# Optimization experiments

Measured on AMD Instinct MI355X. Metric: run time of the kernel, lower is better.

## Reference

```python
import jax, jax.numpy as jnp
import numpy as np

SIGMA = 1.0


def _pairwise_max(q, fact_emb):
    # q: [B, N, D], fact_emb: [F, D]  (D = 3E)
    # Gaussian RBF kernel k(x,y) = exp(-||x-y||^2 / (2*sigma^2)), then max over F.
    q2 = jnp.sum(q * q, axis=-1, keepdims=True)            # [B, N, 1]
    f2 = jnp.sum(fact_emb * fact_emb, axis=-1)             # [F]
    qf = jnp.einsum('bnd,fd->bnf', q, fact_emb)            # [B, N, F]
    d2 = jnp.maximum(q2 + f2[None, None, :] - 2.0 * qf, 0.0)
    k = jnp.exp(-d2 / (2.0 * SIGMA ** 2))                  # [B, N, F]
    return jnp.max(k, axis=2)                              # [B, N]


def setup_inputs() -> dict:
    key = jax.random.key(0)
    ks = jax.random.split(key, 7)
    B, N, F, E = 8, 4000, 4000, 100
    return {
        'rel': jax.random.normal(ks[0], (B, E), jnp.float32),
        'arg1': jax.random.normal(ks[1], (B, E), jnp.float32),
        'arg2': jax.random.normal(ks[2], (B, E), jnp.float32),
        'fact_rel': jax.random.normal(ks[3], (F, E), jnp.float32),
        'fact_arg1': jax.random.normal(ks[4], (F, E), jnp.float32),
        'fact_arg2': jax.random.normal(ks[5], (F, E), jnp.float32),
        'entity_embeddings': jax.random.normal(ks[6], (N, E), jnp.float32),
    }


def reference(rel, arg1, arg2, fact_rel, fact_arg1, fact_arg2, entity_embeddings):
    B = rel.shape[0]
    N, E = entity_embeddings.shape
    fact_emb = jnp.concatenate([fact_rel, fact_arg1, fact_arg2], axis=1)  # [F, 3E]

    rel_b = jnp.broadcast_to(rel[:, None, :], (B, N, E))
    emb_b = jnp.broadcast_to(entity_embeddings[None, :, :], (B, N, E))

    # score_sp: query = [rel, arg1, entity]
    arg1_b = jnp.broadcast_to(arg1[:, None, :], (B, N, E))
    q_sp = jnp.concatenate([rel_b, arg1_b, emb_b], axis=2)  # [B, N, 3E]
    score_sp = _pairwise_max(q_sp, fact_emb)                # [B, N]

    # score_po: query = [rel, entity, arg2]
    arg2_b = jnp.broadcast_to(arg2[:, None, :], (B, N, E))
    q_po = jnp.concatenate([rel_b, emb_b, arg2_b], axis=2)  # [B, N, 3E]
    score_po = _pairwise_max(q_po, fact_emb)                # [B, N]

    return (score_sp, score_po)
```

## Files before the change

### kernel.cpp

```cpp
#include <hip/hip_runtime.h>
#include <math.h>

#define EDIM 100
#define KP   128
#define NF   4000
#define NN   4000
#define NB   8
#define NP   4096
#define BN   128
#define BF   64
#define NFB  (NP / BF)
#define TRS  68

typedef __attribute__((ext_vector_type(8))) short short8;
typedef __attribute__((ext_vector_type(4))) float floatx4;

__device__ __align__(16) unsigned short g_A [NP * KP];
__device__ __align__(16) unsigned short g_B1[NP * KP];
__device__ __align__(16) unsigned short g_B2[NP * KP];
__device__ __align__(16) float g_P[2 * NB * NP];
__device__ float g_e2[NN];
__device__ float g_part[2 * NB * NFB * NP];

__device__ __forceinline__ unsigned short f2bf(float x) {
    union { float f; unsigned int u; } v; v.f = x;
    unsigned int r = v.u + 0x7FFFu + ((v.u >> 16) & 1u);
    return (unsigned short)(r >> 16);
}

__global__ void convert(const float* __restrict__ ent,
                        const float* __restrict__ fa1,
                        const float* __restrict__ fa2) {
    int idx = blockIdx.x * 256 + threadIdx.x;
    const float* src = (blockIdx.y == 0) ? ent : (blockIdx.y == 1) ? fa1 : fa2;
    unsigned short* dst = (blockIdx.y == 0) ? g_A : (blockIdx.y == 1) ? g_B1 : g_B2;
    int row = idx >> 7, k = idx & (KP - 1);
    float v = (row < NF && k < EDIM) ? src[row * EDIM + k] : 0.f;
    dst[idx] = f2bf(v);
}

__global__ void precompute_P(const float* __restrict__ rel,
                             const float* __restrict__ arg1,
                             const float* __restrict__ arg2,
                             const float* __restrict__ frel,
                             const float* __restrict__ fa1,
                             const float* __restrict__ fa2) {
    const int t = threadIdx.x;
    const int fl = t & 15;
    const int kq = t >> 4;
    const int f = blockIdx.x * 16 + fl;
    const int b = blockIdx.y;
    const int fr = (f < NF) ? f : (NF - 1);

    float nf = 0.f, dr = 0.f, d1 = 0.f, d2 = 0.f, qr = 0.f, q1 = 0.f, q2 = 0.f;
    for (int i = 0; i < 25; i++) {
        int k = kq * 25 + i;
        float vr = frel[fr * EDIM + k];
        float v1 = fa1[fr * EDIM + k];
        float v2 = fa2[fr * EDIM + k];
        float rb = rel[b * EDIM + k];
        float a1 = arg1[b * EDIM + k];
        float a2 = arg2[b * EDIM + k];
        nf += vr * vr + v1 * v1 + v2 * v2;
        dr = fmaf(rb, vr, dr);
        d1 = fmaf(a1, v1, d1);
        d2 = fmaf(a2, v2, d2);
        qr = fmaf(rb, rb, qr);
        q1 = fmaf(a1, a1, q1);
        q2 = fmaf(a2, a2, q2);
    }
    nf += __shfl_xor(nf, 16); nf += __shfl_xor(nf, 32);
    dr += __shfl_xor(dr, 16); dr += __shfl_xor(dr, 32);
    d1 += __shfl_xor(d1, 16); d1 += __shfl_xor(d1, 32);
    d2 += __shfl_xor(d2, 16); d2 += __shfl_xor(d2, 32);
    qr += __shfl_xor(qr, 16); qr += __shfl_xor(qr, 32);
    q1 += __shfl_xor(q1, 16); q1 += __shfl_xor(q1, 32);
    q2 += __shfl_xor(q2, 16); q2 += __shfl_xor(q2, 32);
    if (kq == 0) {
        float psp = nf + qr + q1 - 2.f * (dr + d1);
        float ppo = nf + qr + q2 - 2.f * (dr + d2);
        if (f >= NF) { psp = __builtin_inff(); ppo = __builtin_inff(); }
        g_P[(0 * NB + b) * NP + f] = psp;
        g_P[(1 * NB + b) * NP + f] = ppo;
    }
}

__global__ void precompute_e2(const float* __restrict__ ent) {
    int n = blockIdx.x * 256 + threadIdx.x;
    if (n >= NN) return;
    const float4* ep = (const float4*)(ent + n * EDIM);
    float s = 0.f;
    #pragma unroll
    for (int i = 0; i < EDIM / 4; i++) {
        float4 v = ep[i];
        s += v.x * v.x + v.y * v.y + v.z * v.z + v.w * v.w;
    }
    g_e2[n] = s;
}

__global__ void __launch_bounds__(256, 2) main_kernel() {
    __shared__ float4 smem4[4352];
    float4* lA4  = smem4;
    float4* lB14 = smem4 + 2048;
    float4* lB24 = smem4 + 3072;
    float*  tr   = (float*)smem4;

    const int t = threadIdx.x;
    const int n0 = blockIdx.x * BN;
    const int fblk = blockIdx.y;
    const int f0 = fblk * BF;

    const float4* gA4 = (const float4*)g_A;
    const float4* gB14 = (const float4*)g_B1;
    const float4* gB24 = (const float4*)g_B2;
    #pragma unroll
    for (int i = 0; i < 8; i++) {
        int gc = i * 256 + t;
        int row = gc >> 4, ch = gc & 15;
        lA4[row * 16 + (ch ^ (row & 15))] = gA4[n0 * 16 + gc];
    }
    #pragma unroll
    for (int i = 0; i < 4; i++) {
        int gc = i * 256 + t;
        int row = gc >> 4, ch = gc & 15;
        int sl = row * 16 + (ch ^ (row & 15));
        lB14[sl] = gB14[f0 * 16 + gc];
        lB24[sl] = gB24[f0 * 16 + gc];
    }
    __syncthreads();

    const int lane = t & 63;
    const int c = lane & 15;
    const int q = lane >> 4;
    const int w = t >> 6;
    const int w32 = w * 32;

    const short8* pA  = (const short8*)lA4;
    const short8* pB1 = (const short8*)lB14;
    const short8* pB2 = (const short8*)lB24;

    floatx4 acc[2][2][4];
    #pragma unroll
    for (int g = 0; g < 2; g++)
        #pragma unroll
        for (int mt = 0; mt < 2; mt++)
            #pragma unroll
            for (int ft = 0; ft < 4; ft++)
                acc[g][mt][ft] = (floatx4){0.f, 0.f, 0.f, 0.f};

    #pragma unroll
    for (int s = 0; s < 4; s++) {
        const int base = s * 4 + q;
        short8 a0 = pA[(w32 + c) * 16 + (base ^ c)];
        short8 a1 = pA[(w32 + 16 + c) * 16 + (base ^ c)];
        #pragma unroll
        for (int ft = 0; ft < 4; ft++) {
            int sl = (ft * 16 + c) * 16 + (base ^ c);
            short8 b1 = pB1[sl];
            short8 b2 = pB2[sl];
            acc[0][0][ft] = __builtin_amdgcn_mfma_f32_16x16x32_bf16(a0, b2, acc[0][0][ft], 0, 0, 0);
            acc[0][1][ft] = __builtin_amdgcn_mfma_f32_16x16x32_bf16(a1, b2, acc[0][1][ft], 0, 0, 0);
            acc[1][0][ft] = __builtin_amdgcn_mfma_f32_16x16x32_bf16(a0, b1, acc[1][0][ft], 0, 0, 0);
            acc[1][1][ft] = __builtin_amdgcn_mfma_f32_16x16x32_bf16(a1, b1, acc[1][1][ft], 0, 0, 0);
        }
    }

    __syncthreads();

    #pragma unroll
    for (int g = 0; g < 2; g++)
        #pragma unroll
        for (int mt = 0; mt < 2; mt++)
            #pragma unroll
            for (int ft = 0; ft < 4; ft++)
                #pragma unroll
                for (int r = 0; r < 4; r++)
                    tr[(g * BN + w32 + mt * 16 + q * 4 + r) * TRS + ft * 16 + c] =
                        acc[g][mt][ft][r];
    __syncthreads();

    const int g2 = t >> 7;
    const int row = t & 127;
    const float4* trg = (const float4*)(tr + (g2 * BN + row) * TRS);
    float4 G4[16];
    #pragma unroll
    for (int ch = 0; ch < 16; ch++) G4[ch] = trg[ch];

    #pragma unroll
    for (int b = 0; b < NB; b++) {
        const float4* Pp = (const float4*)(g_P + (g2 * NB + b) * NP + f0);
        float4 m4 = {__builtin_inff(), __builtin_inff(), __builtin_inff(), __builtin_inff()};
        #pragma unroll
        for (int ch = 0; ch < 16; ch++) {
            float4 p = Pp[ch];
            m4.x = fminf(m4.x, fmaf(-2.f, G4[ch].x, p.x));
            m4.y = fminf(m4.y, fmaf(-2.f, G4[ch].y, p.y));
            m4.z = fminf(m4.z, fmaf(-2.f, G4[ch].z, p.z));
            m4.w = fminf(m4.w, fmaf(-2.f, G4[ch].w, p.w));
        }
        float m = fminf(fminf(m4.x, m4.y), fminf(m4.z, m4.w));
        g_part[((g2 * NB + b) * NFB + fblk) * NP + n0 + row] = m;
    }
}

__global__ void finalize(float* __restrict__ out) {
    int idx = blockIdx.x * 256 + threadIdx.x;
    if (idx >= 2 * NB * NN) return;
    int sb = idx / NN;
    int n = idx % NN;
    float m = __builtin_inff();
    #pragma unroll 8
    for (int j = 0; j < NFB; j++) m = fminf(m, g_part[(sb * NFB + j) * NP + n]);
    float d2 = fmaxf(m + g_e2[n], 0.f);
    out[idx] = expf(-0.5f * d2);
}

extern "C" void kernel_launch(void* const* d_in, const int* in_sizes, int n_in,
                              void* d_out, int out_size, void* d_ws, size_t ws_size,
                              hipStream_t stream) {
    const float* rel  = (const float*)d_in[0];
    const float* arg1 = (const float*)d_in[1];
    const float* arg2 = (const float*)d_in[2];
    const float* frel = (const float*)d_in[3];
    const float* fa1  = (const float*)d_in[4];
    const float* fa2  = (const float*)d_in[5];
    const float* ent  = (const float*)d_in[6];
    float* out = (float*)d_out;

    convert<<<dim3(NP * KP / 256, 3), 256, 0, stream>>>(ent, fa1, fa2);
    precompute_P<<<dim3(NP / 16, NB), 64, 0, stream>>>(rel, arg1, arg2, frel, fa1, fa2);
    precompute_e2<<<(NN + 255) / 256, 256, 0, stream>>>(ent);
    main_kernel<<<dim3(NP / BN, NFB), 256, 0, stream>>>();
    finalize<<<(2 * NB * NN + 255) / 256, 256, 0, stream>>>(out);
}
```

Before: 136.4 us.

## Fuse prep kernels and loop four F-blocks per main kernel block

The three preprocessing kernels are merged into a single launch that dispatches on block index, which removes two launches. Each main_kernel block now iterates over four F tiles and keeps running minima in registers. This cuts the partial-result buffer and the finalize reduction by a factor of four and stages the P values in shared memory. It still reloads the A tile every iteration, and the grid is four times smaller, which may lower occupancy and parallelism.

```diff
diff --git a/kernel.cpp b/kernel.cpp
--- a/kernel.cpp
+++ b/kernel.cpp
@@ -10,7 +10,13 @@
 #define BN   128
 #define BF   64
 #define NFB  (NP / BF)
+#define FPB  4
+#define NYB  (NFB / FPB)
 #define TRS  68
+
+#define CONVB (3 * (NP * KP / 256))
+#define PREPB ((NP / 64) * NB)
+#define E2B   ((NN + 255) / 256)
 
 typedef __attribute__((ext_vector_type(8))) short short8;
 typedef __attribute__((ext_vector_type(4))) float floatx4;
@@ -20,7 +26,7 @@
 __device__ __align__(16) unsigned short g_B2[NP * KP];
 __device__ __align__(16) float g_P[2 * NB * NP];
 __device__ float g_e2[NN];
-__device__ float g_part[2 * NB * NFB * NP];
+__device__ float g_part[2 * NB * NYB * NP];
 
 __device__ __forceinline__ unsigned short f2bf(float x) {
     union { float f; unsigned int u; } v; v.f = x;
@@ -28,78 +34,81 @@
     return (unsigned short)(r >> 16);
 }
 
-__global__ void convert(const float* __restrict__ ent,
-                        const float* __restrict__ fa1,
-                        const float* __restrict__ fa2) {
-    int idx = blockIdx.x * 256 + threadIdx.x;
-    const float* src = (blockIdx.y == 0) ? ent : (blockIdx.y == 1) ? fa1 : fa2;
-    unsigned short* dst = (blockIdx.y == 0) ? g_A : (blockIdx.y == 1) ? g_B1 : g_B2;
-    int row = idx >> 7, k = idx & (KP - 1);
-    float v = (row < NF && k < EDIM) ? src[row * EDIM + k] : 0.f;
-    dst[idx] = f2bf(v);
-}
-
-__global__ void precompute_P(const float* __restrict__ rel,
-                             const float* __restrict__ arg1,
-                             const float* __restrict__ arg2,
-                             const float* __restrict__ frel,
-                             const float* __restrict__ fa1,
-                             const float* __restrict__ fa2) {
-    const int t = threadIdx.x;
-    const int fl = t & 15;
-    const int kq = t >> 4;
-    const int f = blockIdx.x * 16 + fl;
-    const int b = blockIdx.y;
-    const int fr = (f < NF) ? f : (NF - 1);
-
-    float nf = 0.f, dr = 0.f, d1 = 0.f, d2 = 0.f, qr = 0.f, q1 = 0.f, q2 = 0.f;
-    for (int i = 0; i < 25; i++) {
-        int k = kq * 25 + i;
-        float vr = frel[fr * EDIM + k];
-        float v1 = fa1[fr * EDIM + k];
-        float v2 = fa2[fr * EDIM + k];
-        float rb = rel[b * EDIM + k];
-        float a1 = arg1[b * EDIM + k];
-        float a2 = arg2[b * EDIM + k];
-        nf += vr * vr + v1 * v1 + v2 * v2;
-        dr = fmaf(rb, vr, dr);
-        d1 = fmaf(a1, v1, d1);
-        d2 = fmaf(a2, v2, d2);
-        qr = fmaf(rb, rb, qr);
-        q1 = fmaf(a1, a1, q1);
-        q2 = fmaf(a2, a2, q2);
+__global__ void prep(const float* __restrict__ rel,  const float* __restrict__ arg1,
+                     const float* __restrict__ arg2, const float* __restrict__ frel,
+                     const float* __restrict__ fa1,  const float* __restrict__ fa2,
+                     const float* __restrict__ ent) {
+    const int bx = blockIdx.x;
+    const int t  = threadIdx.x;
+
+    if (bx < CONVB) {
+        int plane = bx / (NP * KP / 256);
+        int idx = (bx - plane * (NP * KP / 256)) * 256 + t;
+        const float* src = (plane == 0) ? ent : (plane == 1) ? fa1 : fa2;
+        unsigned short* dst = (plane == 0) ? g_A : (plane == 1) ? g_B1 : g_B2;
+        int row = idx >> 7, k = idx & (KP - 1);
+        float v = (row < NF && k < EDIM) ? src[row * EDIM + k] : 0.f;
+        dst[idx] = f2bf(v);
+    } else if (bx < CONVB + PREPB) {
+        int pb = bx - CONVB;
+        int b   = pb >> 6;
+        int fbx = pb & 63;
+        int lane = t & 63;
+        int wv = t >> 6;
+        int fl = lane & 15;
+        int kq = lane >> 4;
+        int f = fbx * 64 + wv * 16 + fl;
+        int fr = (f < NF) ? f : (NF - 1);
+
+        float nf = 0.f, dr = 0.f, d1 = 0.f, d2 = 0.f, qr = 0.f, q1 = 0.f, q2 = 0.f;
+        for (int i = 0; i < 25; i++) {
+            int k = kq * 25 + i;
+            float vr = frel[fr * EDIM + k];
+            float v1 = fa1[fr * EDIM + k];
+            float v2 = fa2[fr * EDIM + k];
+            float rb = rel[b * EDIM + k];
+            float a1 = arg1[b * EDIM + k];
+            float a2 = arg2[b * EDIM + k];
+            nf += vr * vr + v1 * v1 + v2 * v2;
+            dr = fmaf(rb, vr, dr);
+            d1 = fmaf(a1, v1, d1);
+            d2 = fmaf(a2, v2, d2);
+            qr = fmaf(rb, rb, qr);
+            q1 = fmaf(a1, a1, q1);
+            q2 = fmaf(a2, a2, q2);
+        }
+        nf += __shfl_xor(nf, 16); nf += __shfl_xor(nf, 32);
+        dr += __shfl_xor(dr, 16); dr += __shfl_xor(dr, 32);
+        d1 += __shfl_xor(d1, 16); d1 += __shfl_xor(d1, 32);
+        d2 += __shfl_xor(d2, 16); d2 += __shfl_xor(d2, 32);
+        qr += __shfl_xor(qr, 16); qr += __shfl_xor(qr, 32);
+        q1 += __shfl_xor(q1, 16); q1 += __shfl_xor(q1, 32);
+        q2 += __shfl_xor(q2, 16); q2 += __shfl_xor(q2, 32);
+        if (kq == 0) {
+            float psp = nf + qr + q1 - 2.f * (dr + d1);
+            float ppo = nf + qr + q2 - 2.f * (dr + d2);
+            if (f >= NF) { psp = __builtin_inff(); ppo = __builtin_inff(); }
+            g_P[(0 * NB + b) * NP + f] = psp;
+            g_P[(1 * NB + b) * NP + f] = ppo;
+        }
+    } else {
+        int n = (bx - CONVB - PREPB) * 256 + t;
+        if (n < NN) {
+            const float4* ep = (const float4*)(ent + n * EDIM);
+            float s = 0.f;
+            #pragma unroll
+            for (int i = 0; i < EDIM / 4; i++) {
+                float4 v = ep[i];
+                s += v.x * v.x + v.y * v.y + v.z * v.z + v.w * v.w;
+            }
+            g_e2[n] = s;
+        }
     }
-    nf += __shfl_xor(nf, 16); nf += __shfl_xor(nf, 32);
-    dr += __shfl_xor(dr, 16); dr += __shfl_xor(dr, 32);
-    d1 += __shfl_xor(d1, 16); d1 += __shfl_xor(d1, 32);
-    d2 += __shfl_xor(d2, 16); d2 += __shfl_xor(d2, 32);
-    qr += __shfl_xor(qr, 16); qr += __shfl_xor(qr, 32);
-    q1 += __shfl_xor(q1, 16); q1 += __shfl_xor(q1, 32);
-    q2 += __shfl_xor(q2, 16); q2 += __shfl_xor(q2, 32);
-    if (kq == 0) {
-        float psp = nf + qr + q1 - 2.f * (dr + d1);
-        float ppo = nf + qr + q2 - 2.f * (dr + d2);
-        if (f >= NF) { psp = __builtin_inff(); ppo = __builtin_inff(); }
-        g_P[(0 * NB + b) * NP + f] = psp;
-        g_P[(1 * NB + b) * NP + f] = ppo;
-    }
-}
-
-__global__ void precompute_e2(const float* __restrict__ ent) {
-    int n = blockIdx.x * 256 + threadIdx.x;
-    if (n >= NN) return;
-    const float4* ep = (const float4*)(ent + n * EDIM);
-    float s = 0.f;
-    #pragma unroll
-    for (int i = 0; i < EDIM / 4; i++) {
-        float4 v = ep[i];
-        s += v.x * v.x + v.y * v.y + v.z * v.z + v.w * v.w;
-    }
-    g_e2[n] = s;
 }
 
 __global__ void __launch_bounds__(256, 2) main_kernel() {
     __shared__ float4 smem4[4352];
+    __shared__ float4 sP4[256];
     float4* lA4  = smem4;
     float4* lB14 = smem4 + 2048;
     float4* lB24 = smem4 + 3072;
@@ -107,100 +116,122 @@
 
     const int t = threadIdx.x;
     const int n0 = blockIdx.x * BN;
-    const int fblk = blockIdx.y;
-    const int f0 = fblk * BF;
-
-    const float4* gA4 = (const float4*)g_A;
-    const float4* gB14 = (const float4*)g_B1;
-    const float4* gB24 = (const float4*)g_B2;
-    #pragma unroll
-    for (int i = 0; i < 8; i++) {
-        int gc = i * 256 + t;
-        int row = gc >> 4, ch = gc & 15;
-        lA4[row * 16 + (ch ^ (row & 15))] = gA4[n0 * 16 + gc];
-    }
-    #pragma unroll
-    for (int i = 0; i < 4; i++) {
-        int gc = i * 256 + t;
-        int row = gc >> 4, ch = gc & 15;
-        int sl = row * 16 + (ch ^ (row & 15));
-        lB14[sl] = gB14[f0 * 16 + gc];
-        lB24[sl] = gB24[f0 * 16 + gc];
-    }
-    __syncthreads();
-
     const int lane = t & 63;
     const int c = lane & 15;
     const int q = lane >> 4;
     const int w = t >> 6;
     const int w32 = w * 32;
-
-    const short8* pA  = (const short8*)lA4;
-    const short8* pB1 = (const short8*)lB14;
-    const short8* pB2 = (const short8*)lB24;
-
-    floatx4 acc[2][2][4];
-    #pragma unroll
-    for (int g = 0; g < 2; g++)
-        #pragma unroll
-        for (int mt = 0; mt < 2; mt++)
-            #pragma unroll
-            for (int ft = 0; ft < 4; ft++)
-                acc[g][mt][ft] = (floatx4){0.f, 0.f, 0.f, 0.f};
-
-    #pragma unroll
-    for (int s = 0; s < 4; s++) {
-        const int base = s * 4 + q;
-        short8 a0 = pA[(w32 + c) * 16 + (base ^ c)];
-        short8 a1 = pA[(w32 + 16 + c) * 16 + (base ^ c)];
-        #pragma unroll
-        for (int ft = 0; ft < 4; ft++) {
-            int sl = (ft * 16 + c) * 16 + (base ^ c);
-            short8 b1 = pB1[sl];
-            short8 b2 = pB2[sl];
-            acc[0][0][ft] = __builtin_amdgcn_mfma_f32_16x16x32_bf16(a0, b2, acc[0][0][ft], 0, 0, 0);
-            acc[0][1][ft] = __builtin_amdgcn_mfma_f32_16x16x32_bf16(a1, b2, acc[0][1][ft], 0, 0, 0);
-            acc[1][0][ft] = __builtin_amdgcn_mfma_f32_16x16x32_bf16(a0, b1, acc[1][0][ft], 0, 0, 0);
-            acc[1][1][ft] = __builtin_amdgcn_mfma_f32_16x16x32_bf16(a1, b1, acc[1][1][ft], 0, 0, 0);
-        }
-    }
-
-    __syncthreads();
-
-    #pragma unroll
-    for (int g = 0; g < 2; g++)
-        #pragma unroll
-        for (int mt = 0; mt < 2; mt++)
-            #pragma unroll
-            for (int ft = 0; ft < 4; ft++)
-                #pragma unroll
-                for (int r = 0; r < 4; r++)
-                    tr[(g * BN + w32 + mt * 16 + q * 4 + r) * TRS + ft * 16 + c] =
-                        acc[g][mt][ft][r];
-    __syncthreads();
-
     const int g2 = t >> 7;
     const int row = t & 127;
-    const float4* trg = (const float4*)(tr + (g2 * BN + row) * TRS);
-    float4 G4[16];
+
+    float m[NB];
     #pragma unroll
-    for (int ch = 0; ch < 16; ch++) G4[ch] = trg[ch];
+    for (int b = 0; b < NB; b++) m[b] = __builtin_inff();
+
+    const float4* gA4  = (const float4*)g_A;
+    const float4* gB14 = (const float4*)g_B1;
+    const float4* gB24 = (const float4*)g_B2;
+
+    #pragma unroll 1
+    for (int ib = 0; ib < FPB; ib++) {
+        const int fblk = blockIdx.y * FPB + ib;
+        const int f0 = fblk * BF;
+
+        #pragma unroll
+        for (int i = 0; i < 8; i++) {
+            int gc = i * 256 + t;
+            int rw = gc >> 4, ch = gc & 15;
+            lA4[rw * 16 + (ch ^ (rw & 15))] = gA4[n0 * 16 + gc];
+        }
+        #pragma unroll
+        for (int i = 0; i < 4; i++) {
+            int gc = i * 256 + t;
+            int rw = gc >> 4, ch = gc & 15;
+            int sl = rw * 16 + (ch ^ (rw & 15));
+            lB14[sl] = gB14[f0 * 16 + gc];
+            lB24[sl] = gB24[f0 * 16 + gc];
+        }
+        {
+            int pg = t >> 7, pb = (t >> 4) & 7, q4 = t & 15;
+            sP4[t] = ((const float4*)(g_P + (pg * NB + pb) * NP + f0))[q4];
+        }
+        __syncthreads();
+
+        const short8* pA  = (const short8*)lA4;
+        const short8* pB1 = (const short8*)lB14;
+        const short8* pB2 = (const short8*)lB24;
+
+        floatx4 acc[2][2][4];
+        #pragma unroll
+        for (int g = 0; g < 2; g++)
+            #pragma unroll
+            for (int mt = 0; mt < 2; mt++)
+                #pragma unroll
+                for (int ft = 0; ft < 4; ft++)
+                    acc[g][mt][ft] = (floatx4){0.f, 0.f, 0.f, 0.f};
+
+        #pragma unroll
+        for (int s = 0; s < 4; s++) {
+            const int base = s * 4 + q;
+            short8 a0 = pA[(w32 + c) * 16 + (base ^ c)];
+            short8 a1 = pA[(w32 + 16 + c) * 16 + (base ^ c)];
+            #pragma unroll
+            for (int ft = 0; ft < 4; ft++) {
+                int sl = (ft * 16 + c) * 16 + (base ^ c);
+                short8 b1 = pB1[sl];
+                short8 b2 = pB2[sl];
+                acc[0][0][ft] = __builtin_amdgcn_mfma_f32_16x16x32_bf16(a0, b2, acc[0][0][ft], 0, 0, 0);
+                acc[0][1][ft] = __builtin_amdgcn_mfma_f32_16x16x32_bf16(a1, b2, acc[0][1][ft], 0, 0, 0);
+                acc[1][0][ft] = __builtin_amdgcn_mfma_f32_16x16x32_bf16(a0, b1, acc[1][0][ft], 0, 0, 0);
+                acc[1][1][ft] = __builtin_amdgcn_mfma_f32_16x16x32_bf16(a1, b1, acc[1][1][ft], 0, 0, 0);
+            }
+        }
+
+        __syncthreads();
+
+        #pragma unroll
+        for (int g = 0; g < 2; g++)
+            #pragma unroll
+            for (int mt = 0; mt < 2; mt++)
+                #pragma unroll
+                for (int ft = 0; ft < 4; ft++)
+                    #pragma unroll
+                    for (int r = 0; r < 4; r++)
+                        tr[(g * BN + w32 + mt * 16 + q * 4 + r) * TRS + ft * 16 + c] =
+                            acc[g][mt][ft][r];
+        __syncthreads();
+
+        const float4* trg = (const float4*)(tr + (g2 * BN + row) * TRS);
+        float4 G4[16];
+        #pragma unroll
+        for (int ch = 0; ch < 16; ch++) G4[ch] = trg[ch];
+
+        #pragma unroll
+        for (int b = 0; b < NB; b++) {
+            const float4* Pl = (const float4*)sP4 + (g2 * NB + b) * 16;
+            float4 m4 = {__builtin_inff(), __builtin_inff(), __builtin_inff(), __builtin_inff()};
+            #pragma unroll
+            for (int ch = 0; ch < 16; ch += 2) {
+                float4 pa = Pl[ch];
+                float4 pb = Pl[ch + 1];
+                float ax = fmaf(-2.f, G4[ch].x, pa.x), bx = fmaf(-2.f, G4[ch + 1].x, pb.x);
+                float ay = fmaf(-2.f, G4[ch].y, pa.y), by = fmaf(-2.f, G4[ch + 1].y, pb.y);
+                float az = fmaf(-2.f, G4[ch].z, pa.z), bz = fmaf(-2.f, G4[ch + 1].z, pb.z);
+                float aw = fmaf(-2.f, G4[ch].w, pa.w), bw = fmaf(-2.f, G4[ch + 1].w, pb.w);
+                m4.x = fminf(m4.x, fminf(ax, bx));
+                m4.y = fminf(m4.y, fminf(ay, by));
+                m4.z = fminf(m4.z, fminf(az, bz));
+                m4.w = fminf(m4.w, fminf(aw, bw));
+            }
+            float mm = fminf(fminf(m4.x, m4.y), fminf(m4.z, m4.w));
+            m[b] = fminf(m[b], mm);
+        }
+        __syncthreads();
+    }
 
     #pragma unroll
-    for (int b = 0; b < NB; b++) {
-        const float4* Pp = (const float4*)(g_P + (g2 * NB + b) * NP + f0);
-        float4 m4 = {__builtin_inff(), __builtin_inff(), __builtin_inff(), __builtin_inff()};
-        #pragma unroll
-        for (int ch = 0; ch < 16; ch++) {
-            float4 p = Pp[ch];
-            m4.x = fminf(m4.x, fmaf(-2.f, G4[ch].x, p.x));
-            m4.y = fminf(m4.y, fmaf(-2.f, G4[ch].y, p.y));
-            m4.z = fminf(m4.z, fmaf(-2.f, G4[ch].z, p.z));
-            m4.w = fminf(m4.w, fmaf(-2.f, G4[ch].w, p.w));
-        }
-        float m = fminf(fminf(m4.x, m4.y), fminf(m4.z, m4.w));
-        g_part[((g2 * NB + b) * NFB + fblk) * NP + n0 + row] = m;
-    }
+    for (int b = 0; b < NB; b++)
+        g_part[((g2 * NB + b) * NYB + blockIdx.y) * NP + n0 + row] = m[b];
 }
 
 __global__ void finalize(float* __restrict__ out) {
@@ -209,8 +240,12 @@
     int sb = idx / NN;
     int n = idx % NN;
     float m = __builtin_inff();
-    #pragma unroll 8
-    for (int j = 0; j < NFB; j++) m = fminf(m, g_part[(sb * NFB + j) * NP + n]);
+    #pragma unroll
+    for (int j = 0; j < NYB; j += 2) {
+        float a = g_part[(sb * NYB + j) * NP + n];
+        float b = g_part[(sb * NYB + j + 1) * NP + n];
+        m = fminf(m, fminf(a, b));
+    }
     float d2 = fmaxf(m + g_e2[n], 0.f);
     out[idx] = expf(-0.5f * d2);
 }
@@ -227,9 +262,7 @@
     const float* ent  = (const float*)d_in[6];
     float* out = (float*)d_out;
 
-    convert<<<dim3(NP * KP / 256, 3), 256, 0, stream>>>(ent, fa1, fa2);
-    precompute_P<<<dim3(NP / 16, NB), 64, 0, stream>>>(rel, arg1, arg2, frel, fa1, fa2);
-    precompute_e2<<<(NN + 255) / 256, 256, 0, stream>>>(ent);
-    main_kernel<<<dim3(NP / BN, NFB), 256, 0, stream>>>();
+    prep<<<dim3(CONVB + PREPB + E2B), 256, 0, stream>>>(rel, arg1, arg2, frel, fa1, fa2, ent);
+    main_kernel<<<dim3(NP / BN, NYB), 256, 0, stream>>>();
     finalize<<<(2 * NB * NN + 255) / 256, 256, 0, stream>>>(out);
 }
```

Result: faster. 133.0 us (-2.5%).
